# Kernel optimization log

Measured on AMD Instinct MI355X. Metric: run time of the kernel, lower is better.

## Reference

```python
import jax, jax.numpy as jnp
import numpy as np

N, C, D, DOUT = 1024, 64, 16, 16   # nodes, channels, irreps_in dim (lmax=3), irreps_out dim
K3, K2, K1 = 16, 8, 4              # CG basis path counts per correlation order
NUM_ELEMENTS = 10


def _sym_basis(key, shape, sym_axes):
    """Random stand-in for e3nn reduced-CG U tensors: symmetrized over input axes."""
    u = jax.random.normal(key, shape, dtype=jnp.float32)
    acc = jnp.zeros(shape, jnp.float32)
    import itertools
    perms = list(itertools.permutations(sym_axes))
    for p in perms:
        order = list(range(len(shape)))
        for a, b in zip(sym_axes, p):
            order[a] = b
        acc = acc + jnp.transpose(u, order)
    return 0.05 * acc / len(perms)


def setup_inputs() -> dict:
    key = jax.random.key(0)
    ks = jax.random.split(key, 8)
    x = jax.random.normal(ks[0], (N, C, D), dtype=jnp.float32)
    indices = jax.random.randint(ks[1], (N,), 0, NUM_ELEMENTS, dtype=jnp.int32)
    w1 = jax.random.normal(ks[2], (NUM_ELEMENTS, K1, C), dtype=jnp.float32)
    w2 = jax.random.normal(ks[3], (NUM_ELEMENTS, K2, C), dtype=jnp.float32)
    w3 = jax.random.normal(ks[4], (NUM_ELEMENTS, K3, C), dtype=jnp.float32)
    U1 = _sym_basis(ks[5], (DOUT, D, K1), (1,))
    U2 = _sym_basis(ks[6], (DOUT, D, D, K2), (1, 2))
    U3 = _sym_basis(ks[7], (DOUT, D, D, D, K3), (1, 2, 3))
    return {"x": x, "indices": indices, "w1": w1, "w2": w2, "w3": w3,
            "U1": U1, "U2": U2, "U3": U3}


def reference(x, indices, w1, w2, w3, U1, U2, U3):
    # Per-node element selection of basis weights (replaces one-hot einsum 'ekc,be->bkc')
    w3s = w3[indices]  # [N, K3, C]
    w2s = w2[indices]  # [N, K2, C]
    w1s = w1[indices]  # [N, K1, C]

    # correlation 3: contract highest-order CG basis with weights and one copy of x
    # out[b,c,o,i,j] = sum_{l,k} U3[o,i,j,l,k] * w3s[b,k,c] * x[b,c,l]
    out = jnp.einsum('oijlk,bkc,bcl->bcoij', U3, w3s, x)

    # correlation 2: add weighted basis, contract one more copy of x
    out = out + jnp.einsum('oijk,bkc->bcoij', U2, w2s)
    out = jnp.einsum('bcoij,bcj->bcoi', out, x)

    # correlation 1: add weighted basis, contract last copy of x
    out = out + jnp.einsum('oik,bkc->bcoi', U1, w1s)
    out = jnp.einsum('bcoi,bci->bco', out, x)  # [N, C, DOUT]
    return out
```

## Files before the change

### kernel.cpp

```cpp
#include <hip/hip_runtime.h>
#include <hip/hip_bf16.h>

#define NCH 64
#define NEL 10
#define NCHUNK 192
#define NSTEP 48
#define NROWS 24576

#define WS_OFFS   0
#define WS_LIST   1024
#define WS_W      2097152

typedef __attribute__((ext_vector_type(8))) short  short8v;
typedef __attribute__((ext_vector_type(4))) float  float4v;
typedef __attribute__((ext_vector_type(4))) int    int4v;

__host__ __device__ constexpr int PJF(int p) { int j = 0; while (p >= j + 1) { p -= j + 1; ++j; } return j; }
__host__ __device__ constexpr int PIF(int p) { int j = 0; while (p >= j + 1) { p -= j + 1; ++j; } return p; }
__host__ __device__ constexpr int PJH(int p) { int j = 8; while (p >= j + 1) { p -= j + 1; ++j; } return j; }
__host__ __device__ constexpr int PIH(int p) { int j = 8; while (p >= j + 1) { p -= j + 1; ++j; } return p; }

__device__ __forceinline__ unsigned int f_to_bf16u(float f) {
  union { float f; unsigned int i; } v; v.f = f;
  unsigned int x = v.i;
  unsigned int r = (x + 0x7fffu + ((x >> 16) & 1u)) >> 16;
  return r & 0xffffu;
}

__global__ __launch_bounds__(256) void k_bgemm(const float* __restrict__ U3,
                                               const float* __restrict__ U2,
                                               const float* __restrict__ U1,
                                               const float* __restrict__ w3,
                                               const float* __restrict__ w2,
                                               const float* __restrict__ w1,
                                               const int* __restrict__ idx,
                                               unsigned short* __restrict__ W,
                                               int* __restrict__ ws_offs,
                                               int* __restrict__ ws_list) {
  __shared__ unsigned short sU[256 * 32];
  __shared__ unsigned short sWt[64 * 32];
  __shared__ char sLT[4][2048];
  __shared__ int cnt[NEL];
  __shared__ int base[NEL + 1];
  int b = blockIdx.x;
  int t = threadIdx.x;

  if (b == 960) {
    if (t < NEL) cnt[t] = 0;
    __syncthreads();
    int mye[4], myp[4];
#pragma unroll
    for (int k = 0; k < 4; ++k) {
      int n = t + k * 256;
      int e = idx[n];
      mye[k] = e;
      myp[k] = atomicAdd(&cnt[e], 1);
    }
    __syncthreads();
    if (t == 0) {
      int a = 0;
      for (int i = 0; i < NEL; ++i) { base[i] = a; a += cnt[i]; }
      base[NEL] = a;
    }
    __syncthreads();
#pragma unroll
    for (int k = 0; k < 4; ++k) ws_list[base[mye[k]] + myp[k]] = t + k * 256;
    if (t <= NEL) ws_offs[t] = base[t];
    return;
  }

  int e = b / 96, rb = b - e * 96;

  {
    int row = rb * 256 + t;
    int o = row / 1536;
    int rem = row - o * 1536;
    int u = rem >> 3, jj = rem & 7;
    int n = u ^ (o & 7);
#pragma unroll
    for (int kq = 0; kq < 4; ++kq) {
      float v[8] = {0.f, 0.f, 0.f, 0.f, 0.f, 0.f, 0.f, 0.f};
      if (n < 172) {
        int ci, cj, h;
        if (n < 72) { int p = n >> 1; h = n & 1; int j = 0; while (p >= j + 1) { p -= j + 1; ++j; } ci = p; cj = j; }
        else        { int p = n - 72; h = 1;     int j = 8; while (p >= j + 1) { p -= j + 1; ++j; } ci = p; cj = j; }
        int l = h * 8 + jj;
        if (kq < 2 && l >= cj) {
          const float* line = U3 + ((((size_t)o * 16 + ci) * 16 + cj) * 16 + l) * 16 + kq * 8;
          float4 q0 = *(const float4*)line;
          float4 q1 = *(const float4*)(line + 4);
          float mult = (ci == cj) ? (cj == l ? 1.f : 3.f) : (cj == l ? 3.f : 6.f);
          v[0] = q0.x * mult; v[1] = q0.y * mult; v[2] = q0.z * mult; v[3] = q0.w * mult;
          v[4] = q1.x * mult; v[5] = q1.y * mult; v[6] = q1.z * mult; v[7] = q1.w * mult;
        }
      } else {
        int r = (n - 172) * 8 + jj;
        if (kq == 2 && r < 136) {
          int p = r, i2 = 0; while (p >= 16 - i2) { p -= 16 - i2; ++i2; }
          int a = i2, bb = i2 + p;
          const float* line = U2 + (((o * 16 + a) * 16) + bb) * 8;
          float4 q0 = *(const float4*)line;
          float4 q1 = *(const float4*)(line + 4);
          float sc = (a == bb) ? 1.f : 2.f;
          v[0] = q0.x * sc; v[1] = q0.y * sc; v[2] = q0.z * sc; v[3] = q0.w * sc;
          v[4] = q1.x * sc; v[5] = q1.y * sc; v[6] = q1.z * sc; v[7] = q1.w * sc;
        } else if (kq == 3 && r >= 136 && r < 152) {
          int a = r - 136;
          float4 q0 = *(const float4*)(U1 + (o * 16 + a) * 4);
          v[0] = q0.x; v[1] = q0.y; v[2] = q0.z; v[3] = q0.w;
        }
      }
      uint4 st;
      st.x = f_to_bf16u(v[0]) | (f_to_bf16u(v[1]) << 16);
      st.y = f_to_bf16u(v[2]) | (f_to_bf16u(v[3]) << 16);
      st.z = f_to_bf16u(v[4]) | (f_to_bf16u(v[5]) << 16);
      st.w = f_to_bf16u(v[6]) | (f_to_bf16u(v[7]) << 16);
      *(uint4*)(&sU[t * 32 + kq * 8]) = st;
    }
  }
  {
    int c = t & 63, kg = t >> 6;
    unsigned int pk[4];
#pragma unroll
    for (int hh = 0; hh < 4; ++hh) {
      int k0 = kg * 8 + hh * 2;
      float f0, f1;
      int k = k0;
      f0 = (k < 16) ? w3[(e * 16 + k) * NCH + c]
         : (k < 24) ? w2[(e * 8 + (k - 16)) * NCH + c]
         : (k < 28) ? w1[(e * 4 + (k - 24)) * NCH + c] : 0.f;
      k = k0 + 1;
      f1 = (k < 16) ? w3[(e * 16 + k) * NCH + c]
         : (k < 24) ? w2[(e * 8 + (k - 16)) * NCH + c]
         : (k < 28) ? w1[(e * 4 + (k - 24)) * NCH + c] : 0.f;
      pk[hh] = f_to_bf16u(f0) | (f_to_bf16u(f1) << 16);
    }
    uint4 st = {pk[0], pk[1], pk[2], pk[3]};
    *(uint4*)(&sWt[c * 32 + kg * 8]) = st;
  }
  __syncthreads();

  int w = t >> 6, lane = t & 63;
  int rc = lane & 15, g = lane >> 4;
  int c = w * 16 + rc;
  short8v bv = *(const short8v*)(sWt + c * 32 + g * 8);
  char* wb = &sLT[w][0];
  int c_r = lane >> 2, q = lane & 3;
  int woff = rc * 128 + ((g * 8) ^ ((rc & 7) << 4));
  int roff0 = c_r * 128 + ((q * 16) ^ ((c_r & 7) << 4));
  int roff1 = c_r * 128 + (((64 + q * 16)) ^ ((c_r & 7) << 4));
  unsigned short* gcol = W + ((size_t)(e * 64 + w * 16 + c_r)) * NROWS + rb * 256;

#pragma unroll 1
  for (int grp = 0; grp < 4; ++grp) {
#pragma unroll
    for (int rt2 = 0; rt2 < 4; ++rt2) {
      int rowL = (grp * 4 + rt2) * 16 + rc;
      short8v av = *(const short8v*)(sU + rowL * 32 + g * 8);
      float4v acc = {0.f, 0.f, 0.f, 0.f};
      acc = __builtin_amdgcn_mfma_f32_16x16x32_bf16(av, bv, acc, 0, 0, 0);
      unsigned int lo, hi;
      asm("v_cvt_pk_bf16_f32 %0, %1, %2" : "=v"(lo) : "v"(acc[0]), "v"(acc[1]));
      asm("v_cvt_pk_bf16_f32 %0, %1, %2" : "=v"(hi) : "v"(acc[2]), "v"(acc[3]));
      uint2 pk = {lo, hi};
      *(uint2*)(wb + (woff ^ (rt2 * 32))) = pk;
    }
    uint4 u0 = *(const uint4*)(wb + roff0);
    uint4 u1 = *(const uint4*)(wb + roff1);
    unsigned short* gp = gcol + grp * 64;
    *(uint4*)(gp + q * 8) = u0;
    *(uint4*)(gp + 32 + q * 8) = u1;
  }
}

#define PACK_MFMA(M0, M1, M2, M3, M4, M5, M6, M7, KK, ACC) { \
  int b0, b1, b2, b3; \
  asm("v_cvt_pk_bf16_f32 %0, %1, %2" : "=v"(b0) : "v"(M0), "v"(M1)); \
  asm("v_cvt_pk_bf16_f32 %0, %1, %2" : "=v"(b1) : "v"(M2), "v"(M3)); \
  asm("v_cvt_pk_bf16_f32 %0, %1, %2" : "=v"(b2) : "v"(M4), "v"(M5)); \
  asm("v_cvt_pk_bf16_f32 %0, %1, %2" : "=v"(b3) : "v"(M6), "v"(M7)); \
  int4v ai = {b0, b1, b2, b3}; \
  short8v av = __builtin_bit_cast(short8v, ai); \
  short8v bv = *(const short8v*)(((KK) & 1 ? bpO : bpE) + ((KK) >> 1) * 128); \
  ACC = __builtin_amdgcn_mfma_f32_16x16x32_bf16(av, bv, ACC, 0, 0, 0); \
}

#define FULL_STEP(KK, ACC) { \
  constexpr int iA = PIF(2 * (KK)), jA = PJF(2 * (KK)); \
  constexpr int iB = PIF(2 * (KK) + 1), jB = PJF(2 * (KK) + 1); \
  float xxA = xr[iA] * xr[jA]; \
  float xxB = xr[iB] * xr[jB]; \
  float xx = selOdd ? xxB : xxA; \
  PACK_MFMA(xx * xsF[0], xx * xsF[1], xx * xsF[2], xx * xsF[3], \
            xx * xsF[4], xx * xsF[5], xx * xsF[6], xx * xsF[7], KK, ACC) \
}

#define H1_STEP(KK, ACC) { \
  constexpr int q = 4 * ((KK) - 18); \
  constexpr int i0 = PIH(q), j0 = PJH(q); \
  constexpr int i1 = PIH(q + 1), j1 = PJH(q + 1); \
  constexpr int i2 = PIH(q + 2), j2 = PJH(q + 2); \
  constexpr int i3 = PIH(q + 3), j3 = PJH(q + 3); \
  float xx0 = xr[i0] * xr[j0], xx1 = xr[i1] * xr[j1]; \
  float xx2 = xr[i2] * xr[j2], xx3 = xr[i3] * xr[j3]; \
  float xxE = selG1 ? xx1 : xx0; \
  float xxO = selG1 ? xx3 : xx2; \
  float xx = selOdd ? xxO : xxE; \
  PACK_MFMA(xx * xr[8], xx * xr[9], xx * xr[10], xx * xr[11], \
            xx * xr[12], xx * xr[13], xx * xr[14], xx * xr[15], KK, ACC) \
}

#define TAIL_STEP(KK, ACC) { \
  float mv[8]; \
  _Pragma("unroll") \
  for (int jj = 0; jj < 8; ++jj) { \
    int spec = sT[((KK) - 43) * 32 + g * 8 + jj]; \
    mv[jj] = sXw[spec & 31] * sXw[(spec >> 8) & 31]; \
  } \
  PACK_MFMA(mv[0], mv[1], mv[2], mv[3], mv[4], mv[5], mv[6], mv[7], KK, ACC) \
}

__global__ __launch_bounds__(512, 4) void k_main(const float* __restrict__ x,
                                                 const int* __restrict__ offs,
                                                 const int* __restrict__ list,
                                                 const unsigned short* __restrict__ W,
                                                 float* __restrict__ out) {
  __shared__ unsigned short sB[16 * NCHUNK * 8];
  __shared__ float sX[8][16][18];
  __shared__ int sT[160];
  int t = threadIdx.x;
  int w = t >> 6, lane = t & 63;
  int rc = lane & 15;
  int g = lane >> 4;
  bool selOdd = g >= 2;
  bool selG1 = g & 1;

  int ec = blockIdx.x;
  int e = ec >> 6, c = ec & 63;

  {
    const uint4* Wg4 = (const uint4*)(W + (size_t)ec * NROWS);
    uint4* sB4 = (uint4*)sB;
#pragma unroll
    for (int s = 0; s < 6; ++s) sB4[t + 512 * s] = Wg4[t + 512 * s];
  }
  if (t < 160) {
    int r = t, a, b;
    if (r < 136) { int p = r, i2 = 0; while (p >= 16 - i2) { p -= 16 - i2; ++i2; } a = i2; b = i2 + p; }
    else if (r < 152) { a = r - 136; b = 16; }
    else { a = 17; b = 17; }
    sT[r] = a | (b << 8);
  }
  __syncthreads();

  float* sXw = &sX[w][rc][0];
  int off = offs[e], nb = offs[e + 1] - off;
  int nt = (nb + 15) >> 4;
  int r2 = (rc >> 2) & 1;
  const char* bpE = (const char*)sB + rc * 3072 + ((g ^ (rc & 3)) + 4 * r2) * 16;
  const char* bpO = (const char*)sB + rc * 3072 + ((g ^ (rc & 3)) + 4 * (1 ^ r2)) * 16;

  for (int tile = w; tile < nt; tile += 8) {
    int m = tile * 16 + rc;
    int node = list[off + (m < nb ? m : nb - 1)];
    float xr[16];
    {
      const float4* xp = (const float4*)(x + ((size_t)node * NCH + c) * 16);
      float4 q0 = xp[0], q1 = xp[1], q2 = xp[2], q3 = xp[3];
      xr[0] = q0.x; xr[1] = q0.y; xr[2] = q0.z; xr[3] = q0.w;
      xr[4] = q1.x; xr[5] = q1.y; xr[6] = q1.z; xr[7] = q1.w;
      xr[8] = q2.x; xr[9] = q2.y; xr[10] = q2.z; xr[11] = q2.w;
      xr[12] = q3.x; xr[13] = q3.y; xr[14] = q3.z; xr[15] = q3.w;
    }
    float xsF[8];
#pragma unroll
    for (int j = 0; j < 8; ++j) xsF[j] = selG1 ? xr[8 + j] : xr[j];
    if (g == 0) {
#pragma unroll
      for (int l = 0; l < 16; ++l) sXw[l] = xr[l];
      sXw[16] = 1.f; sXw[17] = 0.f;
    }

    float4v acc0 = {0.f, 0.f, 0.f, 0.f};
    float4v acc1 = {0.f, 0.f, 0.f, 0.f};
#define S2F(K) FULL_STEP(K, acc0) FULL_STEP((K) + 1, acc1)
#define S2H(K) H1_STEP(K, acc0) H1_STEP((K) + 1, acc1)
    S2F(0) S2F(2) S2F(4) S2F(6) S2F(8) S2F(10) S2F(12) S2F(14) S2F(16)
    S2H(18) S2H(20) S2H(22) S2H(24) S2H(26) S2H(28) S2H(30) S2H(32)
    S2H(34) S2H(36) S2H(38) S2H(40)
    H1_STEP(42, acc0)
    TAIL_STEP(43, acc1)
    TAIL_STEP(44, acc0) TAIL_STEP(45, acc1)
    TAIL_STEP(46, acc0) TAIL_STEP(47, acc1)
    float4v accs = acc0 + acc1;

#pragma unroll
    for (int r3 = 0; r3 < 4; ++r3) {
      int row = g * 4 + r3;
      int mrow = tile * 16 + row;
      if (mrow < nb) {
        int nd = __shfl(node, row);
        out[((size_t)nd * NCH + c) * 16 + rc] = accs[r3];
      }
    }
  }
}

extern "C" void kernel_launch(void* const* d_in, const int* in_sizes, int n_in,
                              void* d_out, int out_size, void* d_ws, size_t ws_size,
                              hipStream_t stream) {
  (void)in_sizes; (void)n_in; (void)out_size; (void)ws_size;
  const float* x   = (const float*)d_in[0];
  const int*   idx = (const int*)d_in[1];
  const float* w1  = (const float*)d_in[2];
  const float* w2  = (const float*)d_in[3];
  const float* w3  = (const float*)d_in[4];
  const float* U1  = (const float*)d_in[5];
  const float* U2  = (const float*)d_in[6];
  const float* U3  = (const float*)d_in[7];
  float* out = (float*)d_out;
  char* ws = (char*)d_ws;
  int* ws_offs = (int*)(ws + WS_OFFS);
  int* ws_list = (int*)(ws + WS_LIST);
  unsigned short* W = (unsigned short*)(ws + WS_W);

  hipLaunchKernelGGL(k_bgemm, dim3(961), dim3(256), 0, stream, U3, U2, U1, w3, w2, w1,
                     idx, W, ws_offs, ws_list);
  hipLaunchKernelGGL(k_main, dim3(640), dim3(512), 0, stream, x, ws_offs, ws_list, W, out);
}
```

Measured before the change: 41.55 us.

## Interleave element blocks across XCDs, async LDS weight load, prefetch first x tile

```diff
diff --git a/kernel.cpp b/kernel.cpp
--- a/kernel.cpp
+++ b/kernel.cpp
@@ -69,7 +69,11 @@
     return;
   }
 
-  int e = b / 96, rb = b - e * 96;
+  int x7 = b & 7, s = b >> 3;
+  int e, rb;
+  if (s < 96)       { e = x7; rb = s; }
+  else if (s < 108) { e = 8;  rb = x7 + 8 * (s - 96); }
+  else              { e = 9;  rb = x7 + 8 * (s - 108); }
 
   {
     int row = rb * 256 + t;
@@ -140,36 +144,38 @@
   }
   __syncthreads();
 
-  int w = t >> 6, lane = t & 63;
-  int rc = lane & 15, g = lane >> 4;
-  int c = w * 16 + rc;
-  short8v bv = *(const short8v*)(sWt + c * 32 + g * 8);
-  char* wb = &sLT[w][0];
-  int c_r = lane >> 2, q = lane & 3;
-  int woff = rc * 128 + ((g * 8) ^ ((rc & 7) << 4));
-  int roff0 = c_r * 128 + ((q * 16) ^ ((c_r & 7) << 4));
-  int roff1 = c_r * 128 + (((64 + q * 16)) ^ ((c_r & 7) << 4));
-  unsigned short* gcol = W + ((size_t)(e * 64 + w * 16 + c_r)) * NROWS + rb * 256;
+  {
+    int w = t >> 6, lane = t & 63;
+    int rc = lane & 15, g = lane >> 4;
+    int c = w * 16 + rc;
+    short8v bv = *(const short8v*)(sWt + c * 32 + g * 8);
+    char* wb = &sLT[w][0];
+    int c_r = lane >> 2, q = lane & 3;
+    int woff = rc * 128 + ((g * 8) ^ ((rc & 7) << 4));
+    int roff0 = c_r * 128 + ((q * 16) ^ ((c_r & 7) << 4));
+    int roff1 = c_r * 128 + (((64 + q * 16)) ^ ((c_r & 7) << 4));
+    unsigned short* gcol = W + ((size_t)(e * 64 + w * 16 + c_r)) * NROWS + rb * 256;
 
 #pragma unroll 1
-  for (int grp = 0; grp < 4; ++grp) {
-#pragma unroll
-    for (int rt2 = 0; rt2 < 4; ++rt2) {
-      int rowL = (grp * 4 + rt2) * 16 + rc;
-      short8v av = *(const short8v*)(sU + rowL * 32 + g * 8);
-      float4v acc = {0.f, 0.f, 0.f, 0.f};
-      acc = __builtin_amdgcn_mfma_f32_16x16x32_bf16(av, bv, acc, 0, 0, 0);
-      unsigned int lo, hi;
-      asm("v_cvt_pk_bf16_f32 %0, %1, %2" : "=v"(lo) : "v"(acc[0]), "v"(acc[1]));
-      asm("v_cvt_pk_bf16_f32 %0, %1, %2" : "=v"(hi) : "v"(acc[2]), "v"(acc[3]));
-      uint2 pk = {lo, hi};
-      *(uint2*)(wb + (woff ^ (rt2 * 32))) = pk;
-    }
-    uint4 u0 = *(const uint4*)(wb + roff0);
-    uint4 u1 = *(const uint4*)(wb + roff1);
-    unsigned short* gp = gcol + grp * 64;
-    *(uint4*)(gp + q * 8) = u0;
-    *(uint4*)(gp + 32 + q * 8) = u1;
+    for (int grp = 0; grp < 4; ++grp) {
+#pragma unroll
+      for (int rt2 = 0; rt2 < 4; ++rt2) {
+        int rowL = (grp * 4 + rt2) * 16 + rc;
+        short8v av = *(const short8v*)(sU + rowL * 32 + g * 8);
+        float4v acc = {0.f, 0.f, 0.f, 0.f};
+        acc = __builtin_amdgcn_mfma_f32_16x16x32_bf16(av, bv, acc, 0, 0, 0);
+        unsigned int lo, hi;
+        asm("v_cvt_pk_bf16_f32 %0, %1, %2" : "=v"(lo) : "v"(acc[0]), "v"(acc[1]));
+        asm("v_cvt_pk_bf16_f32 %0, %1, %2" : "=v"(hi) : "v"(acc[2]), "v"(acc[3]));
+        uint2 pk = {lo, hi};
+        *(uint2*)(wb + (woff ^ (rt2 * 32))) = pk;
+      }
+      uint4 u0 = *(const uint4*)(wb + roff0);
+      uint4 u1 = *(const uint4*)(wb + roff1);
+      unsigned short* gp = gcol + grp * 64;
+      *(uint4*)(gp + q * 8) = u0;
+      *(uint4*)(gp + 32 + q * 8) = u1;
+    }
   }
 }
 
@@ -235,43 +241,62 @@
   bool selOdd = g >= 2;
   bool selG1 = g & 1;
 
-  int ec = blockIdx.x;
-  int e = ec >> 6, c = ec & 63;
-
-  {
-    const uint4* Wg4 = (const uint4*)(W + (size_t)ec * NROWS);
-    uint4* sB4 = (uint4*)sB;
-#pragma unroll
-    for (int s = 0; s < 6; ++s) sB4[t + 512 * s] = Wg4[t + 512 * s];
-  }
-  if (t < 160) {
-    int r = t, a, b;
-    if (r < 136) { int p = r, i2 = 0; while (p >= 16 - i2) { p -= 16 - i2; ++i2; } a = i2; b = i2 + p; }
-    else if (r < 152) { a = r - 136; b = 16; }
-    else { a = 17; b = 17; }
-    sT[r] = a | (b << 8);
-  }
-  __syncthreads();
-
-  float* sXw = &sX[w][rc][0];
+  int b = blockIdx.x;
+  int x7 = b & 7, s = b >> 3;
+  int e, c;
+  if (s < 64)      { e = x7; c = s; }
+  else if (s < 72) { e = 8;  c = x7 + 8 * (s - 64); }
+  else             { e = 9;  c = x7 + 8 * (s - 72); }
+  int ec = e * 64 + c;
+
   int off = offs[e], nb = offs[e + 1] - off;
   int nt = (nb + 15) >> 4;
   int r2 = (rc >> 2) & 1;
   const char* bpE = (const char*)sB + rc * 3072 + ((g ^ (rc & 3)) + 4 * r2) * 16;
   const char* bpO = (const char*)sB + rc * 3072 + ((g ^ (rc & 3)) + 4 * (1 ^ r2)) * 16;
+  float* sXw = &sX[w][rc][0];
+
+  int m0 = w * 16 + rc;
+  int node0 = list[off + (m0 < nb ? m0 : (nb > 0 ? nb - 1 : 0))] & 1023;
+  const float4* xp0 = (const float4*)(x + ((size_t)node0 * NCH + c) * 16);
+  float4 p0 = xp0[0], p1 = xp0[1], p2 = xp0[2], p3 = xp0[3];
+
+  {
+    const uint4* Wg4 = (const uint4*)(W + (size_t)ec * NROWS);
+    uint4* sB4 = (uint4*)sB;
+#pragma unroll
+    for (int s2 = 0; s2 < 6; ++s2) {
+      __builtin_amdgcn_global_load_lds(
+          (const __attribute__((address_space(1))) void*)(Wg4 + t + 512 * s2),
+          (__attribute__((address_space(3))) void*)(sB4 + w * 64 + 512 * s2),
+          16, 0, 0);
+    }
+  }
+  if (t < 160) {
+    int r = t, a, b2;
+    if (r < 136) { int p = r, i2 = 0; while (p >= 16 - i2) { p -= 16 - i2; ++i2; } a = i2; b2 = i2 + p; }
+    else if (r < 152) { a = r - 136; b2 = 16; }
+    else { a = 17; b2 = 17; }
+    sT[r] = a | (b2 << 8);
+  }
+  __syncthreads();
 
   for (int tile = w; tile < nt; tile += 8) {
-    int m = tile * 16 + rc;
-    int node = list[off + (m < nb ? m : nb - 1)];
+    int node;
+    float4 q0, q1, q2, q3;
+    if (tile == w) {
+      node = node0; q0 = p0; q1 = p1; q2 = p2; q3 = p3;
+    } else {
+      int m = tile * 16 + rc;
+      node = list[off + (m < nb ? m : nb - 1)] & 1023;
+      const float4* xp = (const float4*)(x + ((size_t)node * NCH + c) * 16);
+      q0 = xp[0]; q1 = xp[1]; q2 = xp[2]; q3 = xp[3];
+    }
     float xr[16];
-    {
-      const float4* xp = (const float4*)(x + ((size_t)node * NCH + c) * 16);
-      float4 q0 = xp[0], q1 = xp[1], q2 = xp[2], q3 = xp[3];
-      xr[0] = q0.x; xr[1] = q0.y; xr[2] = q0.z; xr[3] = q0.w;
-      xr[4] = q1.x; xr[5] = q1.y; xr[6] = q1.z; xr[7] = q1.w;
-      xr[8] = q2.x; xr[9] = q2.y; xr[10] = q2.z; xr[11] = q2.w;
-      xr[12] = q3.x; xr[13] = q3.y; xr[14] = q3.z; xr[15] = q3.w;
-    }
+    xr[0] = q0.x; xr[1] = q0.y; xr[2] = q0.z; xr[3] = q0.w;
+    xr[4] = q1.x; xr[5] = q1.y; xr[6] = q1.z; xr[7] = q1.w;
+    xr[8] = q2.x; xr[9] = q2.y; xr[10] = q2.z; xr[11] = q2.w;
+    xr[12] = q3.x; xr[13] = q3.y; xr[14] = q3.z; xr[15] = q3.w;
     float xsF[8];
 #pragma unroll
     for (int j = 0; j < 8; ++j) xsF[j] = selG1 ? xr[8 + j] : xr[j];
```

Result: slower. 47.65 us (+14.7%).

## Write basis weights in MFMA-fragment order and read B operands directly from global

Applied to the files above, without the earlier changes.

```diff
diff --git a/kernel.cpp b/kernel.cpp
--- a/kernel.cpp
+++ b/kernel.cpp
@@ -3,9 +3,7 @@
 
 #define NCH 64
 #define NEL 10
-#define NCHUNK 192
 #define NSTEP 48
-#define NROWS 24576
 
 #define WS_OFFS   0
 #define WS_LIST   1024
@@ -34,12 +32,12 @@
                                                const float* __restrict__ w2,
                                                const float* __restrict__ w1,
                                                const int* __restrict__ idx,
-                                               unsigned short* __restrict__ W,
+                                               unsigned short* __restrict__ WK,
                                                int* __restrict__ ws_offs,
                                                int* __restrict__ ws_list) {
   __shared__ unsigned short sU[256 * 32];
   __shared__ unsigned short sWt[64 * 32];
-  __shared__ char sLT[4][2048];
+  __shared__ char sLT[4][8192];
   __shared__ int cnt[NEL];
   __shared__ int base[NEL + 1];
   int b = blockIdx.x;
@@ -69,14 +67,12 @@
     return;
   }
 
-  int e = b / 96, rb = b - e * 96;
+  int e = b / 96, np = b - e * 96;
+  int n0 = np * 2;
 
   {
-    int row = rb * 256 + t;
-    int o = row / 1536;
-    int rem = row - o * 1536;
-    int u = rem >> 3, jj = rem & 7;
-    int n = u ^ (o & 7);
+    int o = t >> 4, dn = (t >> 3) & 1, jj = t & 7;
+    int n = n0 + dn;
 #pragma unroll
     for (int kq = 0; kq < 4; ++kq) {
       float v[8] = {0.f, 0.f, 0.f, 0.f, 0.f, 0.f, 0.f, 0.f};
@@ -140,36 +136,37 @@
   }
   __syncthreads();
 
-  int w = t >> 6, lane = t & 63;
-  int rc = lane & 15, g = lane >> 4;
-  int c = w * 16 + rc;
-  short8v bv = *(const short8v*)(sWt + c * 32 + g * 8);
-  char* wb = &sLT[w][0];
-  int c_r = lane >> 2, q = lane & 3;
-  int woff = rc * 128 + ((g * 8) ^ ((rc & 7) << 4));
-  int roff0 = c_r * 128 + ((q * 16) ^ ((c_r & 7) << 4));
-  int roff1 = c_r * 128 + (((64 + q * 16)) ^ ((c_r & 7) << 4));
-  unsigned short* gcol = W + ((size_t)(e * 64 + w * 16 + c_r)) * NROWS + rb * 256;
+  {
+    int w = t >> 6, lane = t & 63;
+    int rc2 = lane & 15, g2 = lane >> 4;
+    int c = w * 16 + rc2;
+    short8v bv = *(const short8v*)(sWt + c * 32 + g2 * 8);
+    char* wb = &sLT[w][0];
+    int wbyte = rc2 * 512 + (g2 >> 1) * 256 + (g2 & 1) * 8;
 
 #pragma unroll 1
-  for (int grp = 0; grp < 4; ++grp) {
-#pragma unroll
-    for (int rt2 = 0; rt2 < 4; ++rt2) {
-      int rowL = (grp * 4 + rt2) * 16 + rc;
-      short8v av = *(const short8v*)(sU + rowL * 32 + g * 8);
+    for (int rt = 0; rt < 16; ++rt) {
+      short8v av = *(const short8v*)(sU + (rt * 16 + rc2) * 32 + g2 * 8);
       float4v acc = {0.f, 0.f, 0.f, 0.f};
       acc = __builtin_amdgcn_mfma_f32_16x16x32_bf16(av, bv, acc, 0, 0, 0);
       unsigned int lo, hi;
       asm("v_cvt_pk_bf16_f32 %0, %1, %2" : "=v"(lo) : "v"(acc[0]), "v"(acc[1]));
       asm("v_cvt_pk_bf16_f32 %0, %1, %2" : "=v"(hi) : "v"(acc[2]), "v"(acc[3]));
       uint2 pk = {lo, hi};
-      *(uint2*)(wb + (woff ^ (rt2 * 32))) = pk;
-    }
-    uint4 u0 = *(const uint4*)(wb + roff0);
-    uint4 u1 = *(const uint4*)(wb + roff1);
-    unsigned short* gp = gcol + grp * 64;
-    *(uint4*)(gp + q * 8) = u0;
-    *(uint4*)(gp + 32 + q * 8) = u1;
+      *(uint2*)(wb + wbyte + ((rt ^ rc2) & 15) * 16) = pk;
+    }
+    uint4* WK4 = (uint4*)WK;
+    size_t ecw0 = (size_t)(e * 64 + w * 16);
+    int KK0 = n0 >> 2, g0 = n0 & 3;
+#pragma unroll
+    for (int it = 0; it < 8; ++it) {
+      int p = it * 64 + lane;
+      int clocal = p >> 5, i5 = p & 31;
+      int dn = i5 >> 4, o = i5 & 15;
+      uint4 u = *(const uint4*)(wb + clocal * 512 + dn * 256 + ((o ^ clocal) & 15) * 16);
+      size_t unit16 = ((ecw0 + clocal) * 48 + KK0) * 64 + (g0 + dn) * 16 + o;
+      WK4[unit16] = u;
+    }
   }
 }
 
@@ -181,7 +178,7 @@
   asm("v_cvt_pk_bf16_f32 %0, %1, %2" : "=v"(b3) : "v"(M6), "v"(M7)); \
   int4v ai = {b0, b1, b2, b3}; \
   short8v av = __builtin_bit_cast(short8v, ai); \
-  short8v bv = *(const short8v*)(((KK) & 1 ? bpO : bpE) + ((KK) >> 1) * 128); \
+  short8v bv = *(const short8v*)(bk + (KK) * 1024); \
   ACC = __builtin_amdgcn_mfma_f32_16x16x32_bf16(av, bv, ACC, 0, 0, 0); \
 }
 
@@ -220,13 +217,12 @@
   PACK_MFMA(mv[0], mv[1], mv[2], mv[3], mv[4], mv[5], mv[6], mv[7], KK, ACC) \
 }
 
-__global__ __launch_bounds__(512, 4) void k_main(const float* __restrict__ x,
+__global__ __launch_bounds__(256, 4) void k_main(const float* __restrict__ x,
                                                  const int* __restrict__ offs,
                                                  const int* __restrict__ list,
-                                                 const unsigned short* __restrict__ W,
+                                                 const unsigned short* __restrict__ WK,
                                                  float* __restrict__ out) {
-  __shared__ unsigned short sB[16 * NCHUNK * 8];
-  __shared__ float sX[8][16][18];
+  __shared__ float sX[4][16][18];
   __shared__ int sT[160];
   int t = threadIdx.x;
   int w = t >> 6, lane = t & 63;
@@ -235,34 +231,27 @@
   bool selOdd = g >= 2;
   bool selG1 = g & 1;
 
-  int ec = blockIdx.x;
+  int b = blockIdx.x;
+  int ec = b >> 1, half = b & 1;
   int e = ec >> 6, c = ec & 63;
 
-  {
-    const uint4* Wg4 = (const uint4*)(W + (size_t)ec * NROWS);
-    uint4* sB4 = (uint4*)sB;
-#pragma unroll
-    for (int s = 0; s < 6; ++s) sB4[t + 512 * s] = Wg4[t + 512 * s];
-  }
   if (t < 160) {
-    int r = t, a, b;
-    if (r < 136) { int p = r, i2 = 0; while (p >= 16 - i2) { p -= 16 - i2; ++i2; } a = i2; b = i2 + p; }
-    else if (r < 152) { a = r - 136; b = 16; }
-    else { a = 17; b = 17; }
-    sT[r] = a | (b << 8);
+    int r = t, a, b2;
+    if (r < 136) { int p = r, i2 = 0; while (p >= 16 - i2) { p -= 16 - i2; ++i2; } a = i2; b2 = i2 + p; }
+    else if (r < 152) { a = r - 136; b2 = 16; }
+    else { a = 17; b2 = 17; }
+    sT[r] = a | (b2 << 8);
   }
   __syncthreads();
 
   float* sXw = &sX[w][rc][0];
   int off = offs[e], nb = offs[e + 1] - off;
   int nt = (nb + 15) >> 4;
-  int r2 = (rc >> 2) & 1;
-  const char* bpE = (const char*)sB + rc * 3072 + ((g ^ (rc & 3)) + 4 * r2) * 16;
-  const char* bpO = (const char*)sB + rc * 3072 + ((g ^ (rc & 3)) + 4 * (1 ^ r2)) * 16;
-
-  for (int tile = w; tile < nt; tile += 8) {
+  const char* bk = (const char*)WK + (size_t)ec * 49152 + lane * 16;
+
+  for (int tile = half * 4 + w; tile < nt; tile += 8) {
     int m = tile * 16 + rc;
-    int node = list[off + (m < nb ? m : nb - 1)];
+    int node = list[off + (m < nb ? m : nb - 1)] & 1023;
     float xr[16];
     {
       const float4* xp = (const float4*)(x + ((size_t)node * NCH + c) * 16);
@@ -322,9 +311,9 @@
   char* ws = (char*)d_ws;
   int* ws_offs = (int*)(ws + WS_OFFS);
   int* ws_list = (int*)(ws + WS_LIST);
-  unsigned short* W = (unsigned short*)(ws + WS_W);
+  unsigned short* WK = (unsigned short*)(ws + WS_W);
 
   hipLaunchKernelGGL(k_bgemm, dim3(961), dim3(256), 0, stream, U3, U2, U1, w3, w2, w1,
-                     idx, W, ws_offs, ws_list);
-  hipLaunchKernelGGL(k_main, dim3(640), dim3(512), 0, stream, x, ws_offs, ws_list, W, out);
-}
+                     idx, WK, ws_offs, ws_list);
+  hipLaunchKernelGGL(k_main, dim3(1280), dim3(256), 0, stream, x, ws_offs, ws_list, WK, out);
+}
```

Measured after the change: 69.67 us. 67.7% more time.
